# Kernel tuning notes

Measured on AMD Instinct MI355X. Metric: run time of the kernel, lower is better.

Reference implementation:

```python
import jax, jax.numpy as jnp
from jax import lax
import numpy as np

NUM_ANCHORS = 3
NUM_CLASSES = 20
IMG_DIM = 416.0
ANCHORS = np.array([[10.0, 13.0], [16.0, 30.0], [33.0, 23.0]], dtype=np.float32)
BN_EPS = 1e-5


def setup_inputs() -> dict:
    key = jax.random.key(0)
    ks = jax.random.split(key, 8)
    B, Cin, G = 16, 256, 52
    Cmid = 2 * Cin
    Cout = NUM_ANCHORS * (NUM_CLASSES + 5)
    # weights scaled down so exp() in the box decode stays numerically tame
    return {
        "x": jax.random.normal(ks[0], (B, Cin, G, G), jnp.float32),
        "conv1_w": jax.random.normal(ks[1], (Cmid, Cin, 3, 3), jnp.float32) * 0.05,
        "bn_gamma": jnp.ones((Cmid,), jnp.float32),
        "bn_beta": jnp.zeros((Cmid,), jnp.float32),
        "bn_mean": jax.random.normal(ks[2], (Cmid,), jnp.float32) * 0.05,
        "bn_var": jax.random.uniform(ks[3], (Cmid,), jnp.float32, 0.5, 1.5),
        "conv2_w": jax.random.normal(ks[4], (Cout, Cmid, 1, 1), jnp.float32) * 0.05,
        "conv2_b": jnp.zeros((Cout,), jnp.float32),
    }


def _conv(x, w, padding):
    return lax.conv_general_dilated(
        x, w, window_strides=(1, 1), padding=padding,
        dimension_numbers=("NCHW", "OIHW", "NCHW"))


def reference(x, conv1_w, bn_gamma, bn_beta, bn_mean, bn_var, conv2_w, conv2_b):
    # BasicConv: conv3x3 (no bias) -> BatchNorm (inference stats) -> LeakyReLU(0.1)
    y = _conv(x, conv1_w, ((1, 1), (1, 1)))
    inv = bn_gamma / jnp.sqrt(bn_var + BN_EPS)
    y = y * inv[None, :, None, None] + (bn_beta - bn_mean * inv)[None, :, None, None]
    y = jnp.where(y > 0, y, 0.1 * y)
    # 1x1 head conv with bias
    y = _conv(y, conv2_w, ((0, 0), (0, 0))) + conv2_b[None, :, None, None]

    B, G = y.shape[0], y.shape[2]
    A, NC = NUM_ANCHORS, NUM_CLASSES
    # [B, A, 5+NC, G, G] -> [B, A, G, G, 5+NC]
    pred = y.reshape(B, A, NC + 5, G, G).transpose(0, 1, 3, 4, 2)

    obj_score = jax.nn.sigmoid(pred[..., 4])        # [B,A,G,G]
    pred_cls = jax.nn.sigmoid(pred[..., 5:])        # [B,A,G,G,NC]

    stride = IMG_DIM / G
    grid = jnp.arange(G, dtype=jnp.float32)
    grid_x = grid[None, None, None, :]              # [1,1,1,G]
    grid_y = grid[None, None, :, None]              # [1,1,G,1]
    scaled = jnp.asarray(ANCHORS) / stride          # [A,2]
    anchor_w = scaled[:, 0].reshape(1, A, 1, 1)
    anchor_h = scaled[:, 1].reshape(1, A, 1, 1)

    # original uses .data (detached) for box decode
    box_in = lax.stop_gradient(pred[..., :4])
    bx = jax.nn.sigmoid(box_in[..., 0]) + grid_x
    by = jax.nn.sigmoid(box_in[..., 1]) + grid_y
    bw = jnp.exp(box_in[..., 2]) * anchor_w
    bh = jnp.exp(box_in[..., 3]) * anchor_h
    pred_boxes = jnp.stack([bx, by, bw, bh], axis=-1) * stride  # [B,A,G,G,4]

    return jnp.concatenate(
        [pred_boxes.reshape(B, -1, 4),
         obj_score.reshape(B, -1, 1),
         pred_cls.reshape(B, -1, NC)], axis=-1)
```

## Files before the change

### kernel.cpp

```cpp
#include <hip/hip_runtime.h>

typedef _Float16 f16;
typedef _Float16 f16x8 __attribute__((ext_vector_type(8)));
typedef _Float16 f16x4 __attribute__((ext_vector_type(4)));
typedef float f32x4 __attribute__((ext_vector_type(4)));

#define GDIM 52
#define GG 2704
#define CIN 256
#define CMID 512
#define COUT 75
#define NIMG 16
#define SPT 192
#define NSPB 15
#define PH 60
#define PW 54

__device__ __forceinline__ float sigmoidf_(float x) {
    return 1.0f / (1.0f + __expf(-x));
}

__device__ __forceinline__ void gload16(const void* g, void* l) {
    __builtin_amdgcn_global_load_lds(
        (const __attribute__((address_space(1))) unsigned int*)g,
        (__attribute__((address_space(3))) unsigned int*)l, 16, 0, 0);
}

__global__ __launch_bounds__(256) void k_prep_x(const float* __restrict__ x,
                                                f16* __restrict__ x16p) {
    __shared__ float ls[32][133];
    int hw0 = blockIdx.x * 128, ck = blockIdx.y, img = blockIdx.z;
    int tid = threadIdx.x;
    const float* xb = x + ((size_t)img * CIN + ck * 32) * GG;
#pragma unroll
    for (int i = 0; i < 16; ++i) {
        int idx = tid + i * 256;
        int r = idx >> 7, c = idx & 127;
        int hw = hw0 + c;
        ls[r][c] = (hw < GG) ? xb[(size_t)r * GG + hw] : 0.0f;
    }
    __syncthreads();
    int col = tid >> 1, half = tid & 1;
    int hw = hw0 + col;
    if (hw < GG) {
        int h = hw / GDIM, w = hw % GDIM;
        f16* dst = x16p + ((((size_t)img * 8 + ck) * PH + h + 1) * PW + (w + 1)) * 32 + half * 16;
        f16x8 o0, o1;
#pragma unroll
        for (int j = 0; j < 8; ++j) o0[j] = (f16)ls[half * 16 + j][col];
#pragma unroll
        for (int j = 0; j < 8; ++j) o1[j] = (f16)ls[half * 16 + 8 + j][col];
        *(f16x8*)dst = o0;
        *(f16x8*)(dst + 8) = o1;
    }
}

__global__ __launch_bounds__(256) void k_prep_w(
    const float* __restrict__ w1, const float* __restrict__ w2,
    const float* __restrict__ gamma, const float* __restrict__ beta,
    const float* __restrict__ mean, const float* __restrict__ var,
    f16* __restrict__ w16, f16* __restrict__ w2_16,
    float* __restrict__ bnscale, float* __restrict__ bnshift) {
    int i = blockIdx.x * 256 + threadIdx.x;
    int cl = i & 31;
    int co = (i >> 5) & 511;
    int ckt = i >> 14;
    int ck = ckt & 7, tap = ckt >> 3;
    int ci = ck * 32 + cl;
    w16[i] = (f16)w1[(size_t)co * 2304 + ci * 9 + tap];
    if (i < COUT * CMID) w2_16[i] = (f16)w2[i];
    if (i < CMID) {
        float s = gamma[i] * rsqrtf(var[i] + 1e-5f);
        bnscale[i] = s;
        bnshift[i] = beta[i] - mean[i] * s;
    }
}

__global__ __launch_bounds__(512, 2) void k_conv1(
    const f16* __restrict__ x16p, const f16* __restrict__ w16,
    const float* __restrict__ bnscale, const float* __restrict__ bnshift,
    f16* __restrict__ y16) {
    __shared__ __align__(16) f16 At[3][8192];
    __shared__ __align__(16) f16 slab[2][12288];
    int img = blockIdx.x / NSPB, sb = blockIdx.x % NSPB;
    int n0 = sb * SPT;
    int h_lo = n0 / GDIM;
    int co0 = blockIdx.y * 256;
    int tid = threadIdx.x;
    int lane = tid & 63, wave = tid >> 6;
    int wm = wave >> 1, wn = wave & 1;
    int l15 = lane & 15, kg = lane >> 4;

    int roff[6];
#pragma unroll
    for (int nf = 0; nf < 6; ++nf) {
        int n = n0 + wn * 96 + nf * 16 + l15;
        int nc = n < GG ? n : GG - 1;
        int hh = nc / GDIM, ww = nc % GDIM;
        roff[nf] = ((hh - h_lo + 1) * PW + (ww + 1)) * 64 + kg * 16;
    }

    f32x4 acc[4][6];
#pragma unroll
    for (int a = 0; a < 4; ++a)
#pragma unroll
        for (int b = 0; b < 6; ++b) {
            acc[a][b][0] = 0.f; acc[a][b][1] = 0.f;
            acc[a][b][2] = 0.f; acc[a][b][3] = 0.f;
        }

    const f16* xbase = x16p + ((size_t)img * 8 * PH + h_lo) * (PW * 32);

    {
        const f16* wA = w16 + (size_t)co0 * 32;
        gload16(wA + (size_t)tid * 8, &At[0][0] + (size_t)tid * 8);
        gload16(wA + (size_t)(tid + 512) * 8, &At[0][0] + (size_t)(tid + 512) * 8);
        const f16* sg = xbase;
        gload16(sg + (size_t)tid * 8, &slab[0][0] + (size_t)tid * 8);
        gload16(sg + (size_t)(tid + 512) * 8, &slab[0][0] + (size_t)(tid + 512) * 8);
        gload16(sg + (size_t)(tid + 1024) * 8, &slab[0][0] + (size_t)(tid + 1024) * 8);
    }

    for (int ck = 0; ck < 8; ++ck) {
        const char* Sb = (const char*)&slab[ck & 1][0];
#pragma unroll
        for (int tap = 0; tap < 9; ++tap) {
            if (tap == 4 && ck < 7) {
                const f16* sg = xbase + (size_t)(ck + 1) * (PH * PW * 32);
                f16* sd = &slab[(ck + 1) & 1][0];
                gload16(sg + (size_t)tid * 8, sd + (size_t)tid * 8);
                gload16(sg + (size_t)(tid + 512) * 8, sd + (size_t)(tid + 512) * 8);
                gload16(sg + (size_t)(tid + 1024) * 8, sd + (size_t)(tid + 1024) * 8);
            }
            if (!(ck == 7 && tap == 8)) {
                const int tapn = (tap + 1) % 9;
                const int ckn = ck + (tap == 8 ? 1 : 0);
                const f16* wA = w16 + ((size_t)(tapn * 8 + ckn) * 512 + co0) * 32;
                f16* dst = &At[(tap + 1) % 3][0];
                gload16(wA + (size_t)tid * 8, dst + (size_t)tid * 8);
                gload16(wA + (size_t)(tid + 512) * 8, dst + (size_t)(tid + 512) * 8);
            }
            if (ck == 7 && tap == 8)
                asm volatile("s_waitcnt vmcnt(0)" ::: "memory");
            else if (tap == 4 && ck < 7)
                asm volatile("s_waitcnt vmcnt(5)" ::: "memory");
            else
                asm volatile("s_waitcnt vmcnt(2)" ::: "memory");
            __builtin_amdgcn_s_barrier();
            __builtin_amdgcn_sched_barrier(0);
            const f16* Ab = &At[tap % 3][0];
            const int dh = tap / 3 - 1, dw = tap % 3 - 1;
            const int tapadd = (dh * PW + dw) * 64;
            f16x8 af[4], bf[6];
#pragma unroll
            for (int mf = 0; mf < 4; ++mf)
                af[mf] = *(const f16x8*)(Ab + ((wm * 64 + mf * 16 + l15) * 32 + kg * 8));
#pragma unroll
            for (int nf = 0; nf < 6; ++nf)
                bf[nf] = *(const f16x8*)(Sb + (roff[nf] + tapadd));
            __builtin_amdgcn_s_setprio(1);
#pragma unroll
            for (int nf = 0; nf < 6; ++nf)
#pragma unroll
                for (int mf = 0; mf < 4; ++mf)
                    acc[mf][nf] = __builtin_amdgcn_mfma_f32_16x16x32_f16(
                        af[mf], bf[nf], acc[mf][nf], 0, 0, 0);
            __builtin_amdgcn_s_setprio(0);
            __builtin_amdgcn_sched_barrier(0);
        }
    }
#pragma unroll
    for (int mf = 0; mf < 4; ++mf) {
        int cob = co0 + wm * 64 + mf * 16 + kg * 4;
        f32x4 sc = *(const f32x4*)(bnscale + cob);
        f32x4 sh = *(const f32x4*)(bnshift + cob);
#pragma unroll
        for (int nf = 0; nf < 6; ++nf) {
            int n = n0 + wn * 96 + nf * 16 + l15;
            if (n >= GG) continue;
            f16x4 o;
#pragma unroll
            for (int i = 0; i < 4; ++i) {
                float v = acc[mf][nf][i] * sc[i] + sh[i];
                o[i] = (f16)(v > 0.f ? v : 0.1f * v);
            }
            *(f16x4*)(y16 + ((size_t)img * GG + n) * CMID + cob) = o;
        }
    }
}

__global__ __launch_bounds__(256) void k_conv2(
    const f16* __restrict__ y16, const f16* __restrict__ w2_16,
    const float* __restrict__ b2, float* __restrict__ out) {
    __shared__ float ct[128][81];
    int img = blockIdx.x / 22, nb = blockIdx.x % 22;
    int n0 = nb * 128;
    int tid = threadIdx.x;
    int lane = tid & 63, wave = tid >> 6;
    int l15 = lane & 15, kg = lane >> 4;

    f32x4 acc[5][2];
#pragma unroll
    for (int a = 0; a < 5; ++a)
#pragma unroll
        for (int b = 0; b < 2; ++b) {
            acc[a][b][0] = 0.f; acc[a][b][1] = 0.f;
            acc[a][b][2] = 0.f; acc[a][b][3] = 0.f;
        }

    const f16* yb = y16 + (size_t)img * GG * CMID;
    int nn[2];
#pragma unroll
    for (int nf = 0; nf < 2; ++nf) {
        int n = n0 + wave * 32 + nf * 16 + l15;
        nn[nf] = n < GG ? n : GG - 1;
    }
    for (int c0 = 0; c0 < CMID; c0 += 32) {
        f16x8 af[5];
#pragma unroll
        for (int mf = 0; mf < 5; ++mf) {
            int co = mf * 16 + l15;
            if (co < COUT)
                af[mf] = *(const f16x8*)(w2_16 + (size_t)co * CMID + c0 + kg * 8);
            else {
#pragma unroll
                for (int k = 0; k < 8; ++k) af[mf][k] = (f16)0;
            }
        }
#pragma unroll
        for (int nf = 0; nf < 2; ++nf) {
            f16x8 bf = *(const f16x8*)(yb + (size_t)nn[nf] * CMID + c0 + kg * 8);
#pragma unroll
            for (int mf = 0; mf < 5; ++mf)
                acc[mf][nf] = __builtin_amdgcn_mfma_f32_16x16x32_f16(
                    af[mf], bf, acc[mf][nf], 0, 0, 0);
        }
    }
#pragma unroll
    for (int mf = 0; mf < 5; ++mf)
#pragma unroll
        for (int nf = 0; nf < 2; ++nf)
            *(f32x4*)(&ct[wave * 32 + nf * 16 + l15][mf * 16 + kg * 4]) = acc[mf][nf];
    __syncthreads();
    for (int j = tid; j < 384; j += 256) {
        int a = j >> 7, nl = j & 127;
        int n = n0 + nl;
        if (n >= GG) continue;
        const float* t = &ct[nl][a * 25];
        float tv[25];
#pragma unroll
        for (int q = 0; q < 25; ++q) tv[q] = t[q] + b2[a * 25 + q];
        int h = n / GDIM, w = n % GDIM;
        const float AW[3] = {10.f, 16.f, 33.f};
        const float AH[3] = {13.f, 30.f, 23.f};
        float bx = (sigmoidf_(tv[0]) + (float)w) * 8.0f;
        float by = (sigmoidf_(tv[1]) + (float)h) * 8.0f;
        float bw_ = __expf(tv[2]) * AW[a];
        float bh_ = __expf(tv[3]) * AH[a];
        float* o = out + ((size_t)img * 8112 + (size_t)a * GG + n) * 25;
        o[0] = bx; o[1] = by; o[2] = bw_; o[3] = bh_;
        o[4] = sigmoidf_(tv[4]);
#pragma unroll
        for (int q = 0; q < 20; ++q) o[5 + q] = sigmoidf_(tv[5 + q]);
    }
}

extern "C" void kernel_launch(void* const* d_in, const int* in_sizes, int n_in,
                              void* d_out, int out_size, void* d_ws, size_t ws_size,
                              hipStream_t stream) {
    (void)in_sizes; (void)n_in; (void)out_size; (void)ws_size;
    const float* x     = (const float*)d_in[0];
    const float* w1    = (const float*)d_in[1];
    const float* gamma = (const float*)d_in[2];
    const float* beta  = (const float*)d_in[3];
    const float* mean  = (const float*)d_in[4];
    const float* var   = (const float*)d_in[5];
    const float* w2    = (const float*)d_in[6];
    const float* b2    = (const float*)d_in[7];
    float* out = (float*)d_out;

    char* ws = (char*)d_ws;
    f16* x16p     = (f16*)(ws);
    f16* w16      = (f16*)(ws + 26550272);
    f16* w2_16    = (f16*)(ws + 28909568);
    float* bnscale = (float*)(ws + 28986368);
    float* bnshift = (float*)(ws + 28988416);
    f16* y16      = (f16*)(ws + 28990464);

    hipMemsetAsync(x16p, 0, 26542080, stream);
    k_prep_x<<<dim3(22, 8, NIMG), 256, 0, stream>>>(x, x16p);
    k_prep_w<<<4608, 256, 0, stream>>>(w1, w2, gamma, beta, mean, var,
                                       w16, w2_16, bnscale, bnshift);
    k_conv1<<<dim3(NIMG * NSPB, 2), 512, 0, stream>>>(x16p, w16, bnscale,
                                                      bnshift, y16);
    k_conv2<<<NIMG * 22, 256, 0, stream>>>(y16, w2_16, b2, out);
}
```

Measured before the change: 163.7 us.

## Restructure conv1 LDS layouts for conflict-free fragment reads and coalesced output

Rearranges the weight and input slab tiles in shared memory so each k-group of 8 halves sits in its own plane, which is meant to remove bank conflicts on the MFMA fragment loads. The conv1 epilogue now stages the activated tile through LDS and writes y16 in wide coalesced rows. y16 is split into two per-half planes of 256 channels, and conv2 indexing is updated to match. The change also raises the shared-memory footprint to 112 KB per block, which may reduce the number of resident blocks, and it adjusts the vmcnt waits to fit the new load counts.

```diff
diff --git a/kernel.cpp b/kernel.cpp
--- a/kernel.cpp
+++ b/kernel.cpp
@@ -15,6 +15,11 @@
 #define NSPB 15
 #define PH 60
 #define PW 54
+
+#define AT_OFF 0
+#define AT_SZ 16384
+#define SLAB_OFF 49152
+#define SLAB_SZ 32768
 
 __device__ __forceinline__ float sigmoidf_(float x) {
     return 1.0f / (1.0f + __expf(-x));
@@ -80,12 +85,12 @@
     const f16* __restrict__ x16p, const f16* __restrict__ w16,
     const float* __restrict__ bnscale, const float* __restrict__ bnshift,
     f16* __restrict__ y16) {
-    __shared__ __align__(16) f16 At[3][8192];
-    __shared__ __align__(16) f16 slab[2][12288];
+    __shared__ __align__(16) char smem[114688];
     int img = blockIdx.x / NSPB, sb = blockIdx.x % NSPB;
     int n0 = sb * SPT;
     int h_lo = n0 / GDIM;
-    int co0 = blockIdx.y * 256;
+    int half = blockIdx.y;
+    int co0 = half * 256;
     int tid = threadIdx.x;
     int lane = tid & 63, wave = tid >> 6;
     int wm = wave >> 1, wn = wave & 1;
@@ -97,7 +102,7 @@
         int n = n0 + wn * 96 + nf * 16 + l15;
         int nc = n < GG ? n : GG - 1;
         int hh = nc / GDIM, ww = nc % GDIM;
-        roff[nf] = ((hh - h_lo + 1) * PW + (ww + 1)) * 64 + kg * 16;
+        roff[nf] = ((hh - h_lo + 1) * PW + (ww + 1)) * 8;
     }
 
     f32x4 acc[4][6];
@@ -110,54 +115,61 @@
         }
 
     const f16* xbase = x16p + ((size_t)img * 8 * PH + h_lo) * (PW * 32);
+    int spix = tid < 378 ? tid : 377;
 
     {
         const f16* wA = w16 + (size_t)co0 * 32;
-        gload16(wA + (size_t)tid * 8, &At[0][0] + (size_t)tid * 8);
-        gload16(wA + (size_t)(tid + 512) * 8, &At[0][0] + (size_t)(tid + 512) * 8);
-        const f16* sg = xbase;
-        gload16(sg + (size_t)tid * 8, &slab[0][0] + (size_t)tid * 8);
-        gload16(sg + (size_t)(tid + 512) * 8, &slab[0][0] + (size_t)(tid + 512) * 8);
-        gload16(sg + (size_t)(tid + 1024) * 8, &slab[0][0] + (size_t)(tid + 1024) * 8);
+        f16* dst = (f16*)(smem + AT_OFF);
+#pragma unroll
+        for (int p = 0; p < 2; ++p) {
+            int u = p * 512 + tid, s = u >> 8, c = u & 255;
+            gload16(wA + (size_t)c * 32 + s * 8, dst + (size_t)u * 8);
+        }
+        f16* sd = (f16*)(smem + SLAB_OFF);
+#pragma unroll
+        for (int p = 0; p < 4; ++p)
+            gload16(xbase + (size_t)spix * 32 + p * 8, sd + ((size_t)p * 512 + tid) * 8);
     }
 
     for (int ck = 0; ck < 8; ++ck) {
-        const char* Sb = (const char*)&slab[ck & 1][0];
 #pragma unroll
         for (int tap = 0; tap < 9; ++tap) {
-            if (tap == 4 && ck < 7) {
-                const f16* sg = xbase + (size_t)(ck + 1) * (PH * PW * 32);
-                f16* sd = &slab[(ck + 1) & 1][0];
-                gload16(sg + (size_t)tid * 8, sd + (size_t)tid * 8);
-                gload16(sg + (size_t)(tid + 512) * 8, sd + (size_t)(tid + 512) * 8);
-                gload16(sg + (size_t)(tid + 1024) * 8, sd + (size_t)(tid + 1024) * 8);
-            }
             if (!(ck == 7 && tap == 8)) {
                 const int tapn = (tap + 1) % 9;
                 const int ckn = ck + (tap == 8 ? 1 : 0);
                 const f16* wA = w16 + ((size_t)(tapn * 8 + ckn) * 512 + co0) * 32;
-                f16* dst = &At[(tap + 1) % 3][0];
-                gload16(wA + (size_t)tid * 8, dst + (size_t)tid * 8);
-                gload16(wA + (size_t)(tid + 512) * 8, dst + (size_t)(tid + 512) * 8);
+                f16* dst = (f16*)(smem + AT_OFF + ((tap + 1) % 3) * AT_SZ);
+#pragma unroll
+                for (int p = 0; p < 2; ++p) {
+                    int u = p * 512 + tid, s = u >> 8, c = u & 255;
+                    gload16(wA + (size_t)c * 32 + s * 8, dst + (size_t)u * 8);
+                }
+            }
+            if (tap == 4 && ck < 7) {
+                const f16* sg = xbase + (size_t)(ck + 1) * (PH * PW * 32);
+                f16* sd = (f16*)(smem + SLAB_OFF + ((ck + 1) & 1) * SLAB_SZ);
+#pragma unroll
+                for (int p = 0; p < 4; ++p)
+                    gload16(sg + (size_t)spix * 32 + p * 8, sd + ((size_t)p * 512 + tid) * 8);
             }
             if (ck == 7 && tap == 8)
                 asm volatile("s_waitcnt vmcnt(0)" ::: "memory");
-            else if (tap == 4 && ck < 7)
-                asm volatile("s_waitcnt vmcnt(5)" ::: "memory");
+            else if ((tap == 4 || tap == 5) && ck < 7)
+                asm volatile("s_waitcnt vmcnt(6)" ::: "memory");
             else
                 asm volatile("s_waitcnt vmcnt(2)" ::: "memory");
             __builtin_amdgcn_s_barrier();
             __builtin_amdgcn_sched_barrier(0);
-            const f16* Ab = &At[tap % 3][0];
-            const int dh = tap / 3 - 1, dw = tap % 3 - 1;
-            const int tapadd = (dh * PW + dw) * 64;
+            const f16* Ab = (const f16*)(smem + AT_OFF + (tap % 3) * AT_SZ);
+            const f16* Sb = (const f16*)(smem + SLAB_OFF + (ck & 1) * SLAB_SZ);
+            const int tappix = (tap / 3 - 1) * PW + (tap % 3 - 1);
             f16x8 af[4], bf[6];
 #pragma unroll
             for (int mf = 0; mf < 4; ++mf)
-                af[mf] = *(const f16x8*)(Ab + ((wm * 64 + mf * 16 + l15) * 32 + kg * 8));
+                af[mf] = *(const f16x8*)(Ab + kg * 2048 + (wm * 64 + l15) * 8 + mf * 128);
 #pragma unroll
             for (int nf = 0; nf < 6; ++nf)
-                bf[nf] = *(const f16x8*)(Sb + (roff[nf] + tapadd));
+                bf[nf] = *(const f16x8*)(Sb + kg * 4096 + roff[nf] + tappix * 8);
             __builtin_amdgcn_s_setprio(1);
 #pragma unroll
             for (int nf = 0; nf < 6; ++nf)
@@ -169,23 +181,34 @@
             __builtin_amdgcn_sched_barrier(0);
         }
     }
+    __syncthreads();
+    f16* tb = (f16*)smem;
 #pragma unroll
     for (int mf = 0; mf < 4; ++mf) {
-        int cob = co0 + wm * 64 + mf * 16 + kg * 4;
-        f32x4 sc = *(const f32x4*)(bnscale + cob);
-        f32x4 sh = *(const f32x4*)(bnshift + cob);
+        int cr = wm * 64 + mf * 16 + kg * 4;
+        f32x4 sc = *(const f32x4*)(bnscale + co0 + cr);
+        f32x4 sh = *(const f32x4*)(bnshift + co0 + cr);
 #pragma unroll
         for (int nf = 0; nf < 6; ++nf) {
-            int n = n0 + wn * 96 + nf * 16 + l15;
-            if (n >= GG) continue;
+            int pl = wn * 96 + nf * 16 + l15;
             f16x4 o;
 #pragma unroll
             for (int i = 0; i < 4; ++i) {
                 float v = acc[mf][nf][i] * sc[i] + sh[i];
                 o[i] = (f16)(v > 0.f ? v : 0.1f * v);
             }
-            *(f16x4*)(y16 + ((size_t)img * GG + n) * CMID + cob) = o;
-        }
+            *(f16x4*)(tb + pl * 264 + cr) = o;
+        }
+    }
+    __syncthreads();
+    int valid = GG - n0; if (valid > SPT) valid = SPT;
+    f16* yb = y16 + (size_t)half * (NIMG * (size_t)GG * 256) + ((size_t)img * GG + n0) * 256;
+#pragma unroll
+    for (int p = 0; p < 12; ++p) {
+        int u = p * 512 + tid, pl = u >> 5, slot = u & 31;
+        if (pl < valid)
+            *(f16x8*)(yb + (size_t)pl * 256 + slot * 8) =
+                *(const f16x8*)(tb + pl * 264 + slot * 8);
     }
 }
 
@@ -208,7 +231,6 @@
             acc[a][b][2] = 0.f; acc[a][b][3] = 0.f;
         }
 
-    const f16* yb = y16 + (size_t)img * GG * CMID;
     int nn[2];
 #pragma unroll
     for (int nf = 0; nf < 2; ++nf) {
@@ -216,6 +238,9 @@
         nn[nf] = n < GG ? n : GG - 1;
     }
     for (int c0 = 0; c0 < CMID; c0 += 32) {
+        const f16* yb = y16 + (size_t)(c0 >> 8) * (NIMG * (size_t)GG * 256) +
+                        (size_t)img * GG * 256;
+        int c = c0 & 255;
         f16x8 af[5];
 #pragma unroll
         for (int mf = 0; mf < 5; ++mf) {
@@ -229,7 +254,7 @@
         }
 #pragma unroll
         for (int nf = 0; nf < 2; ++nf) {
-            f16x8 bf = *(const f16x8*)(yb + (size_t)nn[nf] * CMID + c0 + kg * 8);
+            f16x8 bf = *(const f16x8*)(yb + (size_t)nn[nf] * 256 + c + kg * 8);
 #pragma unroll
             for (int mf = 0; mf < 5; ++mf)
                 acc[mf][nf] = __builtin_amdgcn_mfma_f32_16x16x32_f16(
@@ -281,11 +306,11 @@
 
     char* ws = (char*)d_ws;
     f16* x16p     = (f16*)(ws);
-    f16* w16      = (f16*)(ws + 26550272);
-    f16* w2_16    = (f16*)(ws + 28909568);
-    float* bnscale = (float*)(ws + 28986368);
-    float* bnshift = (float*)(ws + 28988416);
-    f16* y16      = (f16*)(ws + 28990464);
+    f16* w16      = (f16*)(ws + 26542080);
+    f16* w2_16    = (f16*)(ws + 28901376);
+    float* bnscale = (float*)(ws + 28978176);
+    float* bnshift = (float*)(ws + 28980224);
+    f16* y16      = (f16*)(ws + 28982272);
 
     hipMemsetAsync(x16p, 0, 26542080, stream);
     k_prep_x<<<dim3(22, 8, NIMG), 256, 0, stream>>>(x, x16p);
```

Result: faster. 155.4 us (-5.1%).
